# Kernel optimization log

Measured on AMD Instinct MI355X. Metric: run time of the kernel, lower is better.

## Reference

```python
import jax, jax.numpy as jnp
import numpy as np

B, S, OUT = 256, 256, 64
IN = 4 * S * S


def setup_inputs() -> dict:
    key = jax.random.key(0)
    k1, k2, k3 = jax.random.split(key, 3)
    x = jax.random.normal(k1, (B, IN), dtype=jnp.float32)
    # nn.Linear init scale ~ 1/sqrt(fan_in); exact distribution irrelevant for correctness
    W = jax.random.normal(k2, (OUT, IN), dtype=jnp.float32) * (1.0 / np.sqrt(IN))
    b = jax.random.normal(k3, (OUT,), dtype=jnp.float32) * (1.0 / np.sqrt(IN))
    return {"x": x, "W": W, "b": b}


def _haar_dwt2_features(x):
    # x: [B, 4*S*S] viewed as [B, 4, S, S]; single-level Haar dwt2 per channel.
    # pywt haar: approx=(e+o)/sqrt2, detail=(e-o)/sqrt2 along each axis =>
    # with 2x2 block [[a,b],[c,d]]: LL=(a+b+c+d)/2, cH=(a+b-c-d)/2,
    # cV=(a-b+c-d)/2, cD=(a-b-c+d)/2; code concatenates [LL, cH, cV, cD]
    # per channel, then channels.
    Bn = x.shape[0]
    s = int(np.sqrt(x.shape[1] // 4))
    x4 = x.reshape(Bn, 4, s, s)
    a = x4[:, :, 0::2, 0::2]
    bq = x4[:, :, 0::2, 1::2]
    c = x4[:, :, 1::2, 0::2]
    d = x4[:, :, 1::2, 1::2]
    LL = (a + bq + c + d) * 0.5
    LH = (a + bq - c - d) * 0.5  # pywt cH
    HL = (a - bq + c - d) * 0.5  # pywt cV
    HH = (a - bq - c + d) * 0.5  # pywt cD
    # [B, 4ch, 4subband, s/2, s/2] -> flatten: channel-major, subband next
    t = jnp.stack([LL, LH, HL, HH], axis=2)
    return t.reshape(Bn, -1)


def reference(x, W, b):
    t = _haar_dwt2_features(x)
    # original wraps transform in torch.no_grad()
    t = jax.lax.stop_gradient(t)
    return t @ W.T + b
```

## Files before the change

### kernel.cpp

```cpp
#include <hip/hip_runtime.h>
#include <hip/hip_bf16.h>
#include <stdint.h>


#define IN_K  262144
#define PITCH 264

typedef short bf16x8 __attribute__((ext_vector_type(8)));
typedef float f32x4  __attribute__((ext_vector_type(4)));

__device__ __forceinline__ uint32_t pack2_bf16(float a, float b) {
    uint32_t ua = __float_as_uint(a);
    uint32_t ub = __float_as_uint(b);
    ua = (ua + 0x7fffu + ((ua >> 16) & 1u)) >> 16;
    ub = (ub + 0x7fffu + ((ub >> 16) & 1u)) >> 16;
    return ua | (ub << 16);
}

__global__ __launch_bounds__(512, 4) void wavelet_gemm(
    const float* __restrict__ x, const float* __restrict__ W,
    float* __restrict__ part)
{
    __shared__ short Ash[64 * PITCH];
    __shared__ short Bsh[64 * PITCH];

    const int tid  = threadIdx.x;
    const int lane = tid & 63;
    const int l16  = lane & 15;
    const int l4   = lane >> 4;
    const int wave = tid >> 6;

    const int b    = blockIdx.x;
    const int slot = b >> 3;
    const int mh   = slot & 3;
    const int widx = (b & 7) + 8 * (slot >> 2);
    const int c    = widx >> 5;
    const int ig   = widx & 31;

    const float* xm  = x + (size_t)(mh * 64) * IN_K + c * 65536;
    const float* wcb = W + c * 65536;

    const int a_m  = tid >> 5;
    const int a_j4 = tid & 31;
    const int b_n  = tid >> 4;
    const int b_j  = tid & 15;

    f32x4 af[4][2];
    f32x4 bf[2][4];

    auto load_chunk = [&](int t) {
        const int i  = ig * 4 + (t >> 1);
        const int jh = t & 1;
        const float* xc = xm + 2 * i * 256 + 128 * jh;
#pragma unroll
        for (int r = 0; r < 4; r++) {
            const float* xp = xc + (size_t)(a_m + 16 * r) * IN_K + 4 * a_j4;
            af[r][0] = __builtin_nontemporal_load((const f32x4*)(xp));
            af[r][1] = __builtin_nontemporal_load((const f32x4*)(xp + 256));
        }
        const float* wc = wcb + i * 128 + 64 * jh;
#pragma unroll
        for (int r = 0; r < 2; r++) {
            const float* wp = wc + (size_t)(b_n + 32 * r) * IN_K + 4 * b_j;
            bf[r][0] = *(const f32x4*)(wp);
            bf[r][1] = *(const f32x4*)(wp + 16384);
            bf[r][2] = *(const f32x4*)(wp + 32768);
            bf[r][3] = *(const f32x4*)(wp + 49152);
        }
    };

    auto stage = [&]() {
#pragma unroll
        for (int r = 0; r < 4; r++) {
            const f32x4 f0 = af[r][0], f1 = af[r][1];
            const float s1 = f0[0] + f0[1], d1 = f0[0] - f0[1];
            const float s2 = f1[0] + f1[1], d2 = f1[0] - f1[1];
            const float t1 = f0[2] + f0[3], e1 = f0[2] - f0[3];
            const float t2 = f1[2] + f1[3], e2 = f1[2] - f1[3];
            union { bf16x8 v; uint32_t u[4]; } au;
            au.u[0] = pack2_bf16(s1 + s2, s1 - s2);
            au.u[1] = pack2_bf16(d1 + d2, d1 - d2);
            au.u[2] = pack2_bf16(t1 + t2, t1 - t2);
            au.u[3] = pack2_bf16(e1 + e2, e1 - e2);
            *(bf16x8*)&Ash[(a_m + 16 * r) * PITCH + 8 * a_j4] = au.v;
        }
#pragma unroll
        for (int r = 0; r < 2; r++) {
            const f32x4 v0 = bf[r][0], v1 = bf[r][1];
            const f32x4 v2 = bf[r][2], v3 = bf[r][3];
            union { bf16x8 v; uint32_t u[4]; } b0, b1;
            b0.u[0] = pack2_bf16(v0[0], v1[0]);
            b0.u[1] = pack2_bf16(v2[0], v3[0]);
            b0.u[2] = pack2_bf16(v0[1], v1[1]);
            b0.u[3] = pack2_bf16(v2[1], v3[1]);
            b1.u[0] = pack2_bf16(v0[2], v1[2]);
            b1.u[1] = pack2_bf16(v2[2], v3[2]);
            b1.u[2] = pack2_bf16(v0[3], v1[3]);
            b1.u[3] = pack2_bf16(v2[3], v3[3]);
            short* br = &Bsh[(b_n + 32 * r) * PITCH + 16 * b_j];
            *(bf16x8*)(br)     = b0.v;
            *(bf16x8*)(br + 8) = b1.v;
        }
    };

    const int tm = wave & 3;
    const int nh = wave >> 2;
    f32x4 acc0 = (f32x4){0.f, 0.f, 0.f, 0.f};
    f32x4 acc1 = (f32x4){0.f, 0.f, 0.f, 0.f};

    load_chunk(0);
#pragma unroll 1
    for (int t = 0; t < 8; t++) {
        stage();
        __syncthreads();
        if (t < 7) load_chunk(t + 1);
#pragma unroll
        for (int kh = 0; kh < 8; kh++) {
            const int ko = kh * 32 + l4 * 8;
            bf16x8 a  = *(const bf16x8*)&Ash[(tm * 16 + l16) * PITCH + ko];
            bf16x8 bb0 = *(const bf16x8*)&Bsh[(nh * 32 + l16) * PITCH + ko];
            bf16x8 bb1 = *(const bf16x8*)&Bsh[(nh * 32 + 16 + l16) * PITCH + ko];
            acc0 = __builtin_amdgcn_mfma_f32_16x16x32_bf16(a, bb0, acc0, 0, 0, 0);
            acc1 = __builtin_amdgcn_mfma_f32_16x16x32_bf16(a, bb1, acc1, 0, 0, 0);
        }
        __syncthreads();
    }

    float* pp = part + (size_t)(widx * 4 + mh) * 4096;
#pragma unroll
    for (int r = 0; r < 4; r++) {
        const int m = tm * 16 + l4 * 4 + r;
        __builtin_nontemporal_store(acc0[r], &pp[m * 64 + nh * 32 + l16]);
        __builtin_nontemporal_store(acc1[r], &pp[m * 64 + nh * 32 + 16 + l16]);
    }
}

__global__ __launch_bounds__(512) void wavelet_reduce(
    const float* __restrict__ part, const float* __restrict__ bias,
    float* __restrict__ out)
{
    __shared__ float red[8][64];
    const int m  = blockIdx.x;
    const int mh = m >> 6;
    const int ml = m & 63;
    const int n  = threadIdx.x & 63;
    const int g  = threadIdx.x >> 6;
    const float* base = part + (size_t)mh * 4096 + ml * 64 + n;
    float acc = 0.f;
#pragma unroll 4
    for (int w = g; w < 128; w += 8)
        acc += base[(size_t)w * 16384];
    red[g][n] = acc;
    __syncthreads();
    if (g == 0) {
        const float v = (red[0][n] + red[1][n]) + (red[2][n] + red[3][n])
                      + (red[4][n] + red[5][n]) + (red[6][n] + red[7][n]);
        out[m * 64 + n] = 0.5f * v + bias[n];
    }
}

extern "C" void kernel_launch(void* const* d_in, const int* in_sizes, int n_in,
                              void* d_out, int out_size, void* d_ws, size_t ws_size,
                              hipStream_t stream)
{
    const float* x = (const float*)d_in[0];
    const float* W = (const float*)d_in[1];
    const float* b = (const float*)d_in[2];
    float* out  = (float*)d_out;
    float* part = (float*)d_ws;

    wavelet_gemm<<<512, 512, 0, stream>>>(x, W, part);
    wavelet_reduce<<<256, 512, 0, stream>>>(part, b, out);
}
```

Baseline: 405.4 us.

## Load full 512-float x row-pairs per wave and double-buffer A tile across two chunks

Each wave now loads 8 full rows covering both column halves of a row pair in one contiguous 2KB span per row, instead of splitting the row across two chunks. The Haar-transformed A data for both halves is staged into two shared buffers at once, so A is loaded once per row pair and B is staged twice per iteration. This aims for longer contiguous global reads of x and fewer A load phases. In exchange it doubles A register and LDS footprint, lowering occupancy from 4 to 2 blocks, and adds an extra barrier per iteration.

```diff
diff --git a/kernel.cpp b/kernel.cpp
--- a/kernel.cpp
+++ b/kernel.cpp
@@ -17,11 +17,11 @@
     return ua | (ub << 16);
 }
 
-__global__ __launch_bounds__(512, 4) void wavelet_gemm(
+__global__ __launch_bounds__(512, 2) void wavelet_gemm(
     const float* __restrict__ x, const float* __restrict__ W,
     float* __restrict__ part)
 {
-    __shared__ short Ash[64 * PITCH];
+    __shared__ short Ash[2][64 * PITCH];
     __shared__ short Bsh[64 * PITCH];
 
     const int tid  = threadIdx.x;
@@ -40,24 +40,26 @@
     const float* xm  = x + (size_t)(mh * 64) * IN_K + c * 65536;
     const float* wcb = W + c * 65536;
 
-    const int a_m  = tid >> 5;
-    const int a_j4 = tid & 31;
+    const int a_m0 = wave << 3;
     const int b_n  = tid >> 4;
     const int b_j  = tid & 15;
 
-    f32x4 af[4][2];
+    f32x4 af[8][2];
     f32x4 bf[2][4];
 
-    auto load_chunk = [&](int t) {
-        const int i  = ig * 4 + (t >> 1);
-        const int jh = t & 1;
-        const float* xc = xm + 2 * i * 256 + 128 * jh;
+    auto load_A = [&](int p) {
+        const int i = ig * 4 + p;
 #pragma unroll
-        for (int r = 0; r < 4; r++) {
-            const float* xp = xc + (size_t)(a_m + 16 * r) * IN_K + 4 * a_j4;
+        for (int r = 0; r < 8; r++) {
+            const float* xp = xm + (size_t)(a_m0 + r) * IN_K + 2 * i * 256 + 4 * lane;
             af[r][0] = __builtin_nontemporal_load((const f32x4*)(xp));
             af[r][1] = __builtin_nontemporal_load((const f32x4*)(xp + 256));
         }
+    };
+
+    auto load_B = [&](int t) {
+        const int i  = ig * 4 + (t >> 1);
+        const int jh = t & 1;
         const float* wc = wcb + i * 128 + 64 * jh;
 #pragma unroll
         for (int r = 0; r < 2; r++) {
@@ -69,9 +71,11 @@
         }
     };
 
-    auto stage = [&]() {
+    auto stage_A = [&]() {
+        short* dst = &Ash[lane >> 5][0];
+        const int kofs = 8 * (lane & 31);
 #pragma unroll
-        for (int r = 0; r < 4; r++) {
+        for (int r = 0; r < 8; r++) {
             const f32x4 f0 = af[r][0], f1 = af[r][1];
             const float s1 = f0[0] + f0[1], d1 = f0[0] - f0[1];
             const float s2 = f1[0] + f1[1], d2 = f1[0] - f1[1];
@@ -82,8 +86,11 @@
             au.u[1] = pack2_bf16(d1 + d2, d1 - d2);
             au.u[2] = pack2_bf16(t1 + t2, t1 - t2);
             au.u[3] = pack2_bf16(e1 + e2, e1 - e2);
-            *(bf16x8*)&Ash[(a_m + 16 * r) * PITCH + 8 * a_j4] = au.v;
+            *(bf16x8*)&dst[(a_m0 + r) * PITCH + kofs] = au.v;
         }
+    };
+
+    auto stage_B = [&]() {
 #pragma unroll
         for (int r = 0; r < 2; r++) {
             const f32x4 v0 = bf[r][0], v1 = bf[r][1];
@@ -108,21 +115,33 @@
     f32x4 acc0 = (f32x4){0.f, 0.f, 0.f, 0.f};
     f32x4 acc1 = (f32x4){0.f, 0.f, 0.f, 0.f};
 
-    load_chunk(0);
-#pragma unroll 1
-    for (int t = 0; t < 8; t++) {
-        stage();
-        __syncthreads();
-        if (t < 7) load_chunk(t + 1);
+    auto mfma_chunk = [&](int buf) {
 #pragma unroll
         for (int kh = 0; kh < 8; kh++) {
             const int ko = kh * 32 + l4 * 8;
-            bf16x8 a  = *(const bf16x8*)&Ash[(tm * 16 + l16) * PITCH + ko];
+            bf16x8 a   = *(const bf16x8*)&Ash[buf][(tm * 16 + l16) * PITCH + ko];
             bf16x8 bb0 = *(const bf16x8*)&Bsh[(nh * 32 + l16) * PITCH + ko];
             bf16x8 bb1 = *(const bf16x8*)&Bsh[(nh * 32 + 16 + l16) * PITCH + ko];
             acc0 = __builtin_amdgcn_mfma_f32_16x16x32_bf16(a, bb0, acc0, 0, 0, 0);
             acc1 = __builtin_amdgcn_mfma_f32_16x16x32_bf16(a, bb1, acc1, 0, 0, 0);
         }
+    };
+
+    load_A(0);
+    load_B(0);
+#pragma unroll 1
+    for (int p = 0; p < 4; p++) {
+        stage_A();
+        stage_B();
+        __syncthreads();
+        if (p < 3) load_A(p + 1);
+        load_B(2 * p + 1);
+        mfma_chunk(0);
+        __syncthreads();
+        stage_B();
+        __syncthreads();
+        if (p < 3) load_B(2 * p + 2);
+        mfma_chunk(1);
         __syncthreads();
     }
 
```

Result: no change. 403.5 us (-0.5%).
